# Optimization experiments

Measured on AMD Instinct MI355X. Metric: run time of the kernel, lower is better.

## Reference

```python
import jax, jax.numpy as jnp
import numpy as np

L, N, H, SQ = 24, 16384, 128, 32
D_OP, D_ATTR, D_FILT, D_OUT = 16, 56, 74, 32
D_IN = 2 * SQ + D_OP + D_ATTR  # 136
EPS = 1e-5
SLOPE = 0.01  # LeakyReLU default


def setup_inputs() -> dict:
    key = jax.random.key(0)
    ks = jax.random.split(key, 24)
    f32 = jnp.float32
    inp = {
        'op_pad': jax.random.normal(ks[0], (L, N, D_OP), f32),
        'attr_pad': jax.random.normal(ks[1], (L, N, D_ATTR), f32),
        'filter_pad': jax.random.normal(ks[2], (L, N, D_FILT), f32),
        'output_pad': jax.random.normal(ks[3], (L, N, D_OUT), f32),
        'mapping_pad': jax.random.randint(ks[4], (L, N, 2), 0, N + 1, jnp.int32),
        'batch_size': 4096,
        # filter / output squeeze linears
        'Wf': jax.random.normal(ks[5], (SQ, D_FILT), f32) * 0.05,
        'bf': jax.random.normal(ks[6], (SQ,), f32) * 0.05,
        'Wo': jax.random.normal(ks[7], (SQ, D_OUT), f32) * 0.05,
        'bo': jax.random.normal(ks[8], (SQ,), f32) * 0.05,
        # batchnorm affine params
        'g1': jnp.ones((SQ,), f32), 'beta1': jnp.zeros((SQ,), f32),
        'g2': jnp.ones((SQ,), f32), 'beta2': jnp.zeros((SQ,), f32),
        # LSTM (PyTorch layout: gates i,f,g,o stacked)
        'Wih': jax.random.normal(ks[9], (4 * H, D_IN), f32) * 0.05,
        'Whh': jax.random.normal(ks[10], (4 * H, H), f32) * 0.05,
        'bih': jax.random.normal(ks[11], (4 * H,), f32) * 0.05,
        'bhh': jax.random.normal(ks[12], (4 * H,), f32) * 0.05,
        # final MLP head
        'W1': jax.random.normal(ks[13], (20, H), f32) * 0.05,
        'b1': jax.random.normal(ks[14], (20,), f32) * 0.05,
        'W2': jax.random.normal(ks[15], (1, 20), f32) * 0.05,
        'b2': jax.random.normal(ks[16], (1,), f32) * 0.05,
    }
    return inp


def _leaky(x):
    return jnp.where(x > 0, x, SLOPE * x)


def _bn(x, g, b):
    # BatchNorm1d in training mode: batch stats (biased var), eps=1e-5
    m = jnp.mean(x, axis=0)
    v = jnp.var(x, axis=0)
    return (x - m) * jax.lax.rsqrt(v + EPS) * g + b


def _forward(op_pad, attr_pad, filter_pad, output_pad, mapping_pad, batch_size,
             Wf, bf, Wo, bo, g1, beta1, g2, beta2, Wih, Whh, bih, bhh, W1, b1, W2, b2):
    l, n = op_pad.shape[0], op_pad.shape[1]
    # squeeze filter / output features, flattened over (L*N)
    fd = _bn(_leaky(filter_pad.reshape(l * n, -1) @ Wf.T + bf), g1, beta1).reshape(l, n, SQ)
    od = _bn(_leaky(output_pad.reshape(l * n, -1) @ Wo.T + bo), g2, beta2).reshape(l, n, SQ)
    lstm_in = jnp.concatenate([op_pad, attr_pad, fd, od], axis=2)  # [L,N,D_IN]

    def step(carry, xs):
        h, c = carry                       # [N,H] previous level states
        x, mapping = xs                    # [N,D_IN], [N,2]
        mask = (mapping != 0)[..., None]   # [N,2,1]
        idx = jnp.maximum(mapping - 1, 0)  # [N,2] gather indices
        gh = jnp.sum(jnp.where(mask, h[idx], 0.0), axis=1) * 0.5  # [N,H]
        gc = jnp.sum(jnp.where(mask, c[idx], 0.0), axis=1) * 0.5
        gates = x @ Wih.T + bih + gh @ Whh.T + bhh  # [N,4H]
        i, f, g, o = jnp.split(gates, 4, axis=1)
        c_new = jax.nn.sigmoid(f) * gc + jax.nn.sigmoid(i) * jnp.tanh(g)
        h_new = jax.nn.sigmoid(o) * jnp.tanh(c_new)
        return (h_new, c_new), None

    z = jnp.zeros((n, H), lstm_in.dtype)
    # loop goes from the deepest level (index L-1) up to 0
    (h, _), _ = jax.lax.scan(step, (z, z), (lstm_in[::-1], mapping_pad[::-1]))
    out = h[:batch_size]
    out = jax.nn.sigmoid((out @ W1.T + b1) @ W2.T + b2)  # [B,1]
    return out


def reference(op_pad, attr_pad, filter_pad, output_pad, mapping_pad, batch_size,
              Wf, bf, Wo, bo, g1, beta1, g2, beta2, Wih, Whh, bih, bhh, W1, b1, W2, b2):
    return _forward(op_pad, attr_pad, filter_pad, output_pad, mapping_pad, batch_size,
                    Wf, bf, Wo, bo, g1, beta1, g2, beta2, Wih, Whh, bih, bhh, W1, b1, W2, b2)
```

## Files before the change

### kernel.cpp

```cpp
#include <hip/hip_runtime.h>
#include <hip/hip_bf16.h>

#define LL 24
#define NN 16384
#define HH 128
#define KP 288
#define LN (LL*NN)

typedef __bf16 bf16;
typedef __attribute__((ext_vector_type(8))) __bf16 bf16x8;
typedef __attribute__((ext_vector_type(4))) __bf16 bf16x4;
typedef __attribute__((ext_vector_type(2))) __bf16 bf16x2;
typedef __attribute__((ext_vector_type(4))) float f32x4;

__device__ __forceinline__ float sigm(float x){ return 1.f/(1.f+__expf(-x)); }
__device__ __forceinline__ float tanhfast(float x){
    float e = __expf(-2.f*fabsf(x));
    float t = (1.f-e)/(1.f+e);
    return x >= 0.f ? t : -t;
}
__device__ __forceinline__ void gld16(const void* g, void* l){
    __builtin_amdgcn_global_load_lds(
        (const __attribute__((address_space(1))) void*)g,
        (__attribute__((address_space(3))) void*)l, 16, 0, 0);
}

template<int D, int KQ>
__global__ void prep_wsplit(const float* __restrict__ W, bf16* __restrict__ Wsp)
{
    for (int idx = threadIdx.x; idx < KQ*256; idx += blockDim.x) {
        const int j   = idx & 7;
        const int col = (idx >> 3) & 31;
        const int kq  = idx >> 8;
        const int k   = kq*8 + j;
        float v = (k < D) ? W[col*D + k] : 0.f;
        bf16 h = (bf16)v;
        Wsp[idx]          = h;
        Wsp[KQ*256 + idx] = (bf16)(v - (float)h);
    }
}

template<int D, int KQ, int NQK>
__global__ __launch_bounds__(256) void act_mfma(
    const float* __restrict__ X, const bf16* __restrict__ Wsp,
    const float* __restrict__ bias, bf16* __restrict__ act,
    float* __restrict__ sums)
{
    constexpr int KSTEPS = KQ/4;
    constexpr int TILES  = LN/128;
    __shared__ __align__(16) bf16 XH[KQ*130*8];
    __shared__ __align__(16) bf16 XL[KQ*130*8];
    __shared__ float red[64];
    const int tid  = threadIdx.x;
    const int lane = tid & 63, w = tid >> 6;
    const int l15  = lane & 15, l4 = lane >> 4;

    if (tid < 64) red[tid] = 0.f;

    if constexpr (KQ > NQK) {
        for (int s = tid; s < (KQ-NQK)*128; s += 256) {
            const int kq = NQK + (s >> 7), r = s & 127;
            bf16x8 z;
            #pragma unroll
            for (int j=0;j<8;++j) z[j] = (bf16)0.f;
            *(bf16x8*)&XH[(kq*130 + r)*8] = z;
            *(bf16x8*)&XL[(kq*130 + r)*8] = z;
        }
    }

    bf16x8 wh[KSTEPS][2], wl[KSTEPS][2];
    #pragma unroll
    for (int ks=0; ks<KSTEPS; ++ks)
        #pragma unroll
        for (int cht=0; cht<2; ++cht) {
            const int idx = ((ks*4 + l4)*32 + cht*16 + l15)*8;
            wh[ks][cht] = *(const bf16x8*)&Wsp[idx];
            wl[ks][cht] = *(const bf16x8*)&Wsp[KQ*256 + idx];
        }
    float4 bb[2];
    #pragma unroll
    for (int cht=0; cht<2; ++cht) bb[cht] = *(const float4*)&bias[cht*16 + l4*4];

    float sst[2][4], ssq[2][4];
    #pragma unroll
    for (int c=0;c<2;++c)
        #pragma unroll
        for (int r=0;r<4;++r){ sst[c][r]=0.f; ssq[c][r]=0.f; }

    const int rowb = w*32;
    for (int tile = blockIdx.x; tile < TILES; tile += gridDim.x) {
        __syncthreads();
        const float* Xt = X + (size_t)tile*128*D;
        #pragma unroll
        for (int it = 0; it < (128*NQK)/256; ++it) {
            const int t = it*256 + tid;
            const int r = t / NQK, q = t - r*NQK;
            const float* src = Xt + (size_t)r*D + q*8;
            float xv[8];
            if constexpr (D % 8 != 0) {
                if (q == NQK-1) {
                    #pragma unroll
                    for (int j=0;j<8;++j) xv[j] = (j < D-(NQK-1)*8) ? src[j] : 0.f;
                } else {
                    float2 p0 = *(const float2*)(src);
                    float2 p1 = *(const float2*)(src+2);
                    float2 p2 = *(const float2*)(src+4);
                    float2 p3 = *(const float2*)(src+6);
                    xv[0]=p0.x; xv[1]=p0.y; xv[2]=p1.x; xv[3]=p1.y;
                    xv[4]=p2.x; xv[5]=p2.y; xv[6]=p3.x; xv[7]=p3.y;
                }
            } else {
                float4 f0 = *(const float4*)src;
                float4 f1 = *(const float4*)(src+4);
                xv[0]=f0.x; xv[1]=f0.y; xv[2]=f0.z; xv[3]=f0.w;
                xv[4]=f1.x; xv[5]=f1.y; xv[6]=f1.z; xv[7]=f1.w;
            }
            bf16x8 h8, l8;
            #pragma unroll
            for (int j=0;j<8;++j){
                float x = xv[j];
                bf16 hh = (bf16)x;
                h8[j] = hh;
                l8[j] = (bf16)(x - (float)hh);
            }
            const int slot = (q*130 + r)*8;
            *(bf16x8*)&XH[slot] = h8;
            *(bf16x8*)&XL[slot] = l8;
        }
        __syncthreads();

        f32x4 acc[2][2];
        #pragma unroll
        for (int cht=0; cht<2; ++cht)
            #pragma unroll
            for (int rt=0; rt<2; ++rt)
                acc[cht][rt] = (f32x4){bb[cht].x, bb[cht].y, bb[cht].z, bb[cht].w};

        #pragma unroll
        for (int ks=0; ks<KSTEPS; ++ks) {
            bf16x8 xh[2], xl[2];
            #pragma unroll
            for (int rt=0; rt<2; ++rt) {
                const int slot = ((ks*4 + l4)*130 + rowb + rt*16 + l15)*8;
                xh[rt] = *(const bf16x8*)&XH[slot];
                xl[rt] = *(const bf16x8*)&XL[slot];
            }
            #pragma unroll
            for (int cht=0; cht<2; ++cht)
                #pragma unroll
                for (int rt=0; rt<2; ++rt) {
                    acc[cht][rt] = __builtin_amdgcn_mfma_f32_16x16x32_bf16(
                        wh[ks][cht], xh[rt], acc[cht][rt], 0,0,0);
                    acc[cht][rt] = __builtin_amdgcn_mfma_f32_16x16x32_bf16(
                        wl[ks][cht], xh[rt], acc[cht][rt], 0,0,0);
                    acc[cht][rt] = __builtin_amdgcn_mfma_f32_16x16x32_bf16(
                        wh[ks][cht], xl[rt], acc[cht][rt], 0,0,0);
                }
        }

        #pragma unroll
        for (int cht=0; cht<2; ++cht)
            #pragma unroll
            for (int rt=0; rt<2; ++rt) {
                bf16x4 pk;
                #pragma unroll
                for (int reg=0; reg<4; ++reg) {
                    float u = acc[cht][rt][reg];
                    u = u > 0.f ? u : 0.01f*u;
                    pk[reg] = (bf16)u;
                    sst[cht][reg] += u;
                    ssq[cht][reg] += u*u;
                }
                const long row = (long)tile*128 + rowb + rt*16 + l15;
                *(bf16x4*)&act[row*32 + cht*16 + l4*4] = pk;
            }
    }

    __syncthreads();
    #pragma unroll
    for (int cht=0; cht<2; ++cht)
        #pragma unroll
        for (int reg=0; reg<4; ++reg) {
            const int ch = cht*16 + l4*4 + reg;
            atomicAdd(&red[ch],      sst[cht][reg]);
            atomicAdd(&red[32+ch],   ssq[cht][reg]);
        }
    __syncthreads();
    if (tid < 64) atomicAdd(&sums[tid], red[tid]);
}

__global__ void prep_wtb(const float* __restrict__ Wih, const float* __restrict__ Whh,
                         const float* __restrict__ bih, const float* __restrict__ bhh,
                         bf16* __restrict__ Wtb, float* __restrict__ b4p)
{
    const int np = blockIdx.x;
    const int k  = threadIdx.x;
    const int gate = (np>>4)&3;
    const int j = gate*128 + (np>>6)*16 + (np&15);
    if (k < KP) {
        float v = 0.f;
        if (k < 136)      v = Wih[(long)j*136 + k];
        else if (k >= 160) v = Whh[(long)j*128 + (k-160)];
        Wtb[(long)np*KP + k] = (bf16)v;
    }
    if (k == 0) b4p[np] = bih[j] + bhh[j];
}

__global__ void prep_stats(const float* __restrict__ stats,
    const float* __restrict__ g1, const float* __restrict__ beta1,
    const float* __restrict__ g2, const float* __restrict__ beta2,
    const float* __restrict__ W1, const float* __restrict__ b1,
    const float* __restrict__ W2, const float* __restrict__ b2,
    float* __restrict__ ss, float* __restrict__ wvb)
{
    const int t = threadIdx.x;
    const float inv = 1.f/(float)LN;
    if (t < 32) {
        float mean = stats[t]*inv;
        float var  = stats[32+t]*inv - mean*mean;
        float sc = g1[t]/sqrtf(var + 1e-5f);
        ss[t] = sc; ss[32+t] = beta1[t] - mean*sc;
    } else if (t < 64) {
        int c = t - 32;
        float mean = stats[64+c]*inv;
        float var  = stats[96+c]*inv - mean*mean;
        float sc = g2[c]/sqrtf(var + 1e-5f);
        ss[64+c] = sc; ss[96+c] = beta2[c] - mean*sc;
    }
    float s = 0.f;
    for (int a=0;a<20;++a) s += W2[a]*W1[a*HH + t];
    wvb[t] = s;
    if (t == 0) {
        float sb = 0.f;
        for (int a=0;a<20;++a) sb += W2[a]*b1[a];
        wvb[128] = sb + b2[0];
    }
}

__global__ __launch_bounds__(256) void build_a(
    const float* __restrict__ op, const float* __restrict__ attr,
    const bf16* __restrict__ actf, const bf16* __restrict__ acto,
    const int* __restrict__ map, const float* __restrict__ ss,
    const bf16* __restrict__ h_prev, bf16* __restrict__ A,
    int l, int first)
{
    const int n0 = blockIdx.x * 32;
    const long lbase = (long)l * NN;
    for (int i = threadIdx.x; i < 32*36; i += 256) {
        const int r = i / 36, c = i - r*36;
        const long n = n0 + r;
        const long e = lbase + n;
        const int k0 = c*8;
        bf16x8 out;
        if (c < 9) {
            const float* src = (c < 2) ? (op + e*16 + k0) : (attr + e*56 + (k0-16));
            float4 f0 = *(const float4*)src;
            float4 f1 = *(const float4*)(src+4);
            out[0]=(bf16)f0.x; out[1]=(bf16)f0.y; out[2]=(bf16)f0.z; out[3]=(bf16)f0.w;
            out[4]=(bf16)f1.x; out[5]=(bf16)f1.y; out[6]=(bf16)f1.z; out[7]=(bf16)f1.w;
        } else if (c < 17) {
            const int ch = (c < 13) ? (k0-72) : (k0-104);
            const bf16* src = (c < 13) ? (actf + e*32 + ch) : (acto + e*32 + ch);
            const float* s = ss + ((c < 13) ? 0 : 64);
            bf16x8 v = *(const bf16x8*)src;
            #pragma unroll
            for (int j=0;j<8;++j)
                out[j] = (bf16)fmaf((float)v[j], s[ch+j], s[32+ch+j]);
        } else if (c < 20) {
            #pragma unroll
            for (int j=0;j<8;++j) out[j] = (bf16)0.f;
        } else {
            const int jj = k0 - 160;
            float g[8] = {0,0,0,0,0,0,0,0};
            if (!first) {
                int2 mp = *(const int2*)&map[e*2];
                if (mp.x) { bf16x8 v = *(const bf16x8*)&h_prev[(long)(mp.x-1)*HH + jj];
                    #pragma unroll
                    for (int j=0;j<8;++j) g[j] += (float)v[j]; }
                if (mp.y) { bf16x8 v = *(const bf16x8*)&h_prev[(long)(mp.y-1)*HH + jj];
                    #pragma unroll
                    for (int j=0;j<8;++j) g[j] += (float)v[j]; }
            }
            #pragma unroll
            for (int j=0;j<8;++j) out[j] = (bf16)(0.5f*g[j]);
        }
        *(bf16x8*)&A[n*KP + k0] = out;
    }
}

__global__ __launch_bounds__(256) void lstm_gemm(
    const bf16* __restrict__ A, const bf16* __restrict__ Wtb,
    const float* __restrict__ b4p, const int* __restrict__ map,
    const float* __restrict__ c_prev, float* __restrict__ c_next,
    bf16* __restrict__ h_next, int l, int first)
{
    __shared__ bf16 As[128*32];
    __shared__ bf16 Bs[128*32];
    const int tid  = threadIdx.x;
    const int bm   = blockIdx.x;
    const int bn   = blockIdx.y;
    const int m0   = bm*128, n0p = bn*128;
    const int lane = tid & 63, w = tid >> 6;
    const int wr   = w >> 1,  wc = w & 1;

    f32x4 acc[4][4];
    #pragma unroll
    for (int ni=0; ni<4; ++ni){
        float b = b4p[n0p + wc*64 + ni*16 + (lane&15)];
        #pragma unroll
        for (int mi=0; mi<4; ++mi) acc[mi][ni] = (f32x4){b,b,b,b};
    }

    const bf16* Ab = A   + (size_t)m0*KP;
    const bf16* Bb = Wtb + (size_t)n0p*KP;
    const int lrr = lane >> 2;
    const int qs  = lane & 3;

    for (int kk=0; kk<9; ++kk){
        __syncthreads();
        #pragma unroll
        for (int hh=0; hh<2; ++hh){
            const int lr = w*32 + hh*16 + lrr;
            const int q  = qs ^ ((lr>>1)&3);
            const size_t go = (size_t)lr*KP + kk*32 + q*8;
            gld16(Ab + go, &As[(w*32 + hh*16)*32]);
            gld16(Bb + go, &Bs[(w*32 + hh*16)*32]);
        }
        __syncthreads();
        bf16x8 af[4], bfr[4];
        #pragma unroll
        for (int t4=0; t4<4; ++t4){
            const int am = wr*64 + t4*16 + (lane&15);
            af[t4] = *(const bf16x8*)&As[am*32 + (((lane>>4) ^ ((am>>1)&3))<<3)];
            const int bn_ = wc*64 + t4*16 + (lane&15);
            bfr[t4] = *(const bf16x8*)&Bs[bn_*32 + (((lane>>4) ^ ((bn_>>1)&3))<<3)];
        }
        #pragma unroll
        for (int mi=0; mi<4; ++mi)
            #pragma unroll
            for (int ni=0; ni<4; ++ni)
                acc[mi][ni] = __builtin_amdgcn_mfma_f32_16x16x32_bf16(
                    af[mi], bfr[ni], acc[mi][ni], 0, 0, 0);
    }

    const long lbase = (long)l * NN;
    const int cell = bn*32 + wc*16 + (lane&15);
    #pragma unroll
    for (int mi=0; mi<4; ++mi){
        const int rbase = m0 + wr*64 + mi*16 + (lane>>4)*4;
        #pragma unroll
        for (int reg=0; reg<4; ++reg){
            const int n = rbase + reg;
            float gc = 0.f;
            if (!first){
                int2 mp = *(const int2*)&map[(lbase+n)*2];
                if (mp.x) gc += c_prev[(long)(mp.x-1)*HH + cell];
                if (mp.y) gc += c_prev[(long)(mp.y-1)*HH + cell];
                gc *= 0.5f;
            }
            float cn = sigm(acc[mi][1][reg])*gc
                     + sigm(acc[mi][0][reg])*tanhfast(acc[mi][2][reg]);
            float hn = sigm(acc[mi][3][reg])*tanhfast(cn);
            c_next[(long)n*HH + cell] = cn;
            h_next[(long)n*HH + cell] = (bf16)hn;
        }
    }
}

__global__ __launch_bounds__(256) void final_k(
    const bf16* __restrict__ h, const float* __restrict__ wvb,
    float* __restrict__ out, int rows)
{
    int gt = blockIdx.x*256 + threadIdx.x;
    int row = gt >> 6;
    int lane = gt & 63;
    if (row >= rows) return;
    float v = fmaf((float)h[(long)row*HH + lane], wvb[lane],
                   (float)h[(long)row*HH + 64 + lane] * wvb[64+lane]);
    #pragma unroll
    for (int off=32; off>0; off>>=1) v += __shfl_down(v, off);
    if (lane == 0) out[row] = sigm(v + wvb[128]);
}

extern "C" void kernel_launch(void* const* d_in, const int* in_sizes, int n_in,
                              void* d_out, int out_size, void* d_ws, size_t ws_size,
                              hipStream_t stream)
{
    const float* op      = (const float*)d_in[0];
    const float* attr    = (const float*)d_in[1];
    const float* filt    = (const float*)d_in[2];
    const float* outp    = (const float*)d_in[3];
    const int*   mapping = (const int*)d_in[4];
    const float* Wf  = (const float*)d_in[6];
    const float* bf_ = (const float*)d_in[7];
    const float* Wo  = (const float*)d_in[8];
    const float* bo  = (const float*)d_in[9];
    const float* g1  = (const float*)d_in[10];
    const float* be1 = (const float*)d_in[11];
    const float* g2  = (const float*)d_in[12];
    const float* be2 = (const float*)d_in[13];
    const float* Wih = (const float*)d_in[14];
    const float* Whh = (const float*)d_in[15];
    const float* bih = (const float*)d_in[16];
    const float* bhh = (const float*)d_in[17];
    const float* W1  = (const float*)d_in[18];
    const float* b1  = (const float*)d_in[19];
    const float* W2  = (const float*)d_in[20];
    const float* b2  = (const float*)d_in[21];

    char* p = (char*)d_ws;
    auto alloc = [&](size_t bytes){ char* r = p; p += (bytes + 255) & ~255ull; return r; };
    bf16* actf = (bf16*)alloc((size_t)LN*32*2);
    bf16* acto = (bf16*)alloc((size_t)LN*32*2);
    bf16* h0   = (bf16*)alloc((size_t)NN*HH*2);
    bf16* h1   = (bf16*)alloc((size_t)NN*HH*2);
    float* c0  = (float*)alloc((size_t)NN*HH*4);
    float* c1  = (float*)alloc((size_t)NN*HH*4);
    bf16* Abuf = (bf16*)alloc((size_t)NN*KP*2);
    bf16* Wtb  = (bf16*)alloc((size_t)512*KP*2);
    float* b4p = (float*)alloc(512*4);
    float* stats=(float*)alloc(128*4);
    float* ssb = (float*)alloc(128*4);
    float* wvb = (float*)alloc(132*4);
    bf16* wspf = (bf16*)alloc((size_t)12*256*2*2);
    bf16* wspo = (bf16*)alloc((size_t)4*256*2*2);

    hipMemsetAsync(stats, 0, 128*sizeof(float), stream);
    prep_wsplit<74,12><<<1, 256, 0, stream>>>(Wf, wspf);
    prep_wsplit<32, 4><<<1, 256, 0, stream>>>(Wo, wspo);
    act_mfma<74,12,10><<<768, 256, 0, stream>>>(filt, wspf, bf_, actf, stats);
    act_mfma<32, 4, 4><<<1536, 256, 0, stream>>>(outp, wspo, bo, acto, stats+64);
    prep_wtb<<<512, 320, 0, stream>>>(Wih, Whh, bih, bhh, Wtb, b4p);
    prep_stats<<<1, 128, 0, stream>>>(stats, g1, be1, g2, be2, W1, b1, W2, b2, ssb, wvb);

    bf16*  hb[2] = {h0, h1};
    float* cb[2] = {c0, c1};
    for (int t = 0; t < LL; ++t) {
        const int l = (LL-1) - t;
        const int first = (t == 0);
        build_a<<<NN/32, 256, 0, stream>>>(op, attr, actf, acto, mapping, ssb,
                                           hb[t&1], Abuf, l, first);
        lstm_gemm<<<dim3(128,4), 256, 0, stream>>>(Abuf, Wtb, b4p, mapping,
            cb[t&1], cb[(t+1)&1], hb[(t+1)&1], l, first);
    }
    final_k<<<(out_size*64 + 255)/256, 256, 0, stream>>>(hb[0], wvb, (float*)d_out, out_size);
}
```

Measured before the change: 1.321 ms.

## Fuse LSTM input gather into GEMM, fold BN into weights, drop LDS staging

The per-level build_a kernel and its A buffer are removed. lstm_fused now loads op/attr/activation fragments and gathers child h states directly into MFMA operand registers, skipping the K-steps for h on the first level. The batchnorm scale and shift are folded into the Wih columns and the bias inside prep_wtb, which now runs after prep_stats. The squeeze-linear kernels also drop LDS staging and have each wave load its 16-row tile straight from global memory. This removes a global round trip and one launch per level, at the cost of uncoalesced direct global loads in the GEMM with no LDS reuse of the weights.

```diff
diff --git a/kernel.cpp b/kernel.cpp
--- a/kernel.cpp
+++ b/kernel.cpp
@@ -10,7 +10,6 @@
 typedef __bf16 bf16;
 typedef __attribute__((ext_vector_type(8))) __bf16 bf16x8;
 typedef __attribute__((ext_vector_type(4))) __bf16 bf16x4;
-typedef __attribute__((ext_vector_type(2))) __bf16 bf16x2;
 typedef __attribute__((ext_vector_type(4))) float f32x4;
 
 __device__ __forceinline__ float sigm(float x){ return 1.f/(1.f+__expf(-x)); }
@@ -18,11 +17,6 @@
     float e = __expf(-2.f*fabsf(x));
     float t = (1.f-e)/(1.f+e);
     return x >= 0.f ? t : -t;
-}
-__device__ __forceinline__ void gld16(const void* g, void* l){
-    __builtin_amdgcn_global_load_lds(
-        (const __attribute__((address_space(1))) void*)g,
-        (__attribute__((address_space(3))) void*)l, 16, 0, 0);
 }
 
 template<int D, int KQ>
@@ -40,16 +34,13 @@
     }
 }
 
-template<int D, int KQ, int NQK>
-__global__ __launch_bounds__(256) void act_mfma(
+template<int D, int KSTEPS>
+__global__ __launch_bounds__(256) void act_direct(
     const float* __restrict__ X, const bf16* __restrict__ Wsp,
     const float* __restrict__ bias, bf16* __restrict__ act,
     float* __restrict__ sums)
 {
-    constexpr int KSTEPS = KQ/4;
-    constexpr int TILES  = LN/128;
-    __shared__ __align__(16) bf16 XH[KQ*130*8];
-    __shared__ __align__(16) bf16 XL[KQ*130*8];
+    constexpr int KQ = KSTEPS*4;
     __shared__ float red[64];
     const int tid  = threadIdx.x;
     const int lane = tid & 63, w = tid >> 6;
@@ -57,17 +48,6 @@
 
     if (tid < 64) red[tid] = 0.f;
 
-    if constexpr (KQ > NQK) {
-        for (int s = tid; s < (KQ-NQK)*128; s += 256) {
-            const int kq = NQK + (s >> 7), r = s & 127;
-            bf16x8 z;
-            #pragma unroll
-            for (int j=0;j<8;++j) z[j] = (bf16)0.f;
-            *(bf16x8*)&XH[(kq*130 + r)*8] = z;
-            *(bf16x8*)&XL[(kq*130 + r)*8] = z;
-        }
-    }
-
     bf16x8 wh[KSTEPS][2], wl[KSTEPS][2];
     #pragma unroll
     for (int ks=0; ks<KSTEPS; ++ks)
@@ -87,93 +67,68 @@
         #pragma unroll
         for (int r=0;r<4;++r){ sst[c][r]=0.f; ssq[c][r]=0.f; }
 
-    const int rowb = w*32;
-    for (int tile = blockIdx.x; tile < TILES; tile += gridDim.x) {
-        __syncthreads();
-        const float* Xt = X + (size_t)tile*128*D;
-        #pragma unroll
-        for (int it = 0; it < (128*NQK)/256; ++it) {
-            const int t = it*256 + tid;
-            const int r = t / NQK, q = t - r*NQK;
-            const float* src = Xt + (size_t)r*D + q*8;
+    const int gw = blockIdx.x*4 + w, nw = gridDim.x*4;
+    for (int tile = gw; tile < LN/16; tile += nw) {
+        const long row = (long)tile*16 + l15;
+        const float* xp = X + row*D;
+
+        f32x4 acc[2];
+        #pragma unroll
+        for (int cht=0; cht<2; ++cht)
+            acc[cht] = (f32x4){bb[cht].x, bb[cht].y, bb[cht].z, bb[cht].w};
+
+        #pragma unroll
+        for (int ks=0; ks<KSTEPS; ++ks) {
+            const int k0 = ks*32 + l4*8;
             float xv[8];
-            if constexpr (D % 8 != 0) {
-                if (q == NQK-1) {
-                    #pragma unroll
-                    for (int j=0;j<8;++j) xv[j] = (j < D-(NQK-1)*8) ? src[j] : 0.f;
-                } else {
-                    float2 p0 = *(const float2*)(src);
-                    float2 p1 = *(const float2*)(src+2);
-                    float2 p2 = *(const float2*)(src+4);
-                    float2 p3 = *(const float2*)(src+6);
+            if constexpr (D % 32 == 0) {
+                float4 a = *(const float4*)(xp + k0);
+                float4 b = *(const float4*)(xp + k0 + 4);
+                xv[0]=a.x; xv[1]=a.y; xv[2]=a.z; xv[3]=a.w;
+                xv[4]=b.x; xv[5]=b.y; xv[6]=b.z; xv[7]=b.w;
+            } else {
+                const int rem = D - k0;
+                if (rem >= 8) {
+                    float2 p0 = *(const float2*)(xp + k0);
+                    float2 p1 = *(const float2*)(xp + k0 + 2);
+                    float2 p2 = *(const float2*)(xp + k0 + 4);
+                    float2 p3 = *(const float2*)(xp + k0 + 6);
                     xv[0]=p0.x; xv[1]=p0.y; xv[2]=p1.x; xv[3]=p1.y;
                     xv[4]=p2.x; xv[5]=p2.y; xv[6]=p3.x; xv[7]=p3.y;
+                } else {
+                    #pragma unroll
+                    for (int j=0;j<8;++j) xv[j] = (j < rem) ? xp[k0+j] : 0.f;
                 }
-            } else {
-                float4 f0 = *(const float4*)src;
-                float4 f1 = *(const float4*)(src+4);
-                xv[0]=f0.x; xv[1]=f0.y; xv[2]=f0.z; xv[3]=f0.w;
-                xv[4]=f1.x; xv[5]=f1.y; xv[6]=f1.z; xv[7]=f1.w;
-            }
-            bf16x8 h8, l8;
+            }
+            bf16x8 xh, xl;
             #pragma unroll
             for (int j=0;j<8;++j){
                 float x = xv[j];
                 bf16 hh = (bf16)x;
-                h8[j] = hh;
-                l8[j] = (bf16)(x - (float)hh);
-            }
-            const int slot = (q*130 + r)*8;
-            *(bf16x8*)&XH[slot] = h8;
-            *(bf16x8*)&XL[slot] = l8;
-        }
-        __syncthreads();
-
-        f32x4 acc[2][2];
-        #pragma unroll
-        for (int cht=0; cht<2; ++cht)
+                xh[j] = hh;
+                xl[j] = (bf16)(x - (float)hh);
+            }
             #pragma unroll
-            for (int rt=0; rt<2; ++rt)
-                acc[cht][rt] = (f32x4){bb[cht].x, bb[cht].y, bb[cht].z, bb[cht].w};
-
-        #pragma unroll
-        for (int ks=0; ks<KSTEPS; ++ks) {
-            bf16x8 xh[2], xl[2];
+            for (int cht=0; cht<2; ++cht) {
+                acc[cht] = __builtin_amdgcn_mfma_f32_16x16x32_bf16(wh[ks][cht], xh, acc[cht], 0,0,0);
+                acc[cht] = __builtin_amdgcn_mfma_f32_16x16x32_bf16(wl[ks][cht], xh, acc[cht], 0,0,0);
+                acc[cht] = __builtin_amdgcn_mfma_f32_16x16x32_bf16(wh[ks][cht], xl, acc[cht], 0,0,0);
+            }
+        }
+
+        #pragma unroll
+        for (int cht=0; cht<2; ++cht) {
+            bf16x4 pk;
             #pragma unroll
-            for (int rt=0; rt<2; ++rt) {
-                const int slot = ((ks*4 + l4)*130 + rowb + rt*16 + l15)*8;
-                xh[rt] = *(const bf16x8*)&XH[slot];
-                xl[rt] = *(const bf16x8*)&XL[slot];
-            }
-            #pragma unroll
-            for (int cht=0; cht<2; ++cht)
-                #pragma unroll
-                for (int rt=0; rt<2; ++rt) {
-                    acc[cht][rt] = __builtin_amdgcn_mfma_f32_16x16x32_bf16(
-                        wh[ks][cht], xh[rt], acc[cht][rt], 0,0,0);
-                    acc[cht][rt] = __builtin_amdgcn_mfma_f32_16x16x32_bf16(
-                        wl[ks][cht], xh[rt], acc[cht][rt], 0,0,0);
-                    acc[cht][rt] = __builtin_amdgcn_mfma_f32_16x16x32_bf16(
-                        wh[ks][cht], xl[rt], acc[cht][rt], 0,0,0);
-                }
-        }
-
-        #pragma unroll
-        for (int cht=0; cht<2; ++cht)
-            #pragma unroll
-            for (int rt=0; rt<2; ++rt) {
-                bf16x4 pk;
-                #pragma unroll
-                for (int reg=0; reg<4; ++reg) {
-                    float u = acc[cht][rt][reg];
-                    u = u > 0.f ? u : 0.01f*u;
-                    pk[reg] = (bf16)u;
-                    sst[cht][reg] += u;
-                    ssq[cht][reg] += u*u;
-                }
-                const long row = (long)tile*128 + rowb + rt*16 + l15;
-                *(bf16x4*)&act[row*32 + cht*16 + l4*4] = pk;
-            }
+            for (int reg=0; reg<4; ++reg) {
+                float u = acc[cht][reg];
+                u = u > 0.f ? u : 0.01f*u;
+                pk[reg] = (bf16)u;
+                sst[cht][reg] += u;
+                ssq[cht][reg] += u*u;
+            }
+            *(bf16x4*)&act[row*32 + cht*16 + l4*4] = pk;
+        }
     }
 
     __syncthreads();
@@ -182,28 +137,11 @@
         #pragma unroll
         for (int reg=0; reg<4; ++reg) {
             const int ch = cht*16 + l4*4 + reg;
-            atomicAdd(&red[ch],      sst[cht][reg]);
-            atomicAdd(&red[32+ch],   ssq[cht][reg]);
+            atomicAdd(&red[ch],    sst[cht][reg]);
+            atomicAdd(&red[32+ch], ssq[cht][reg]);
         }
     __syncthreads();
     if (tid < 64) atomicAdd(&sums[tid], red[tid]);
-}
-
-__global__ void prep_wtb(const float* __restrict__ Wih, const float* __restrict__ Whh,
-                         const float* __restrict__ bih, const float* __restrict__ bhh,
-                         bf16* __restrict__ Wtb, float* __restrict__ b4p)
-{
-    const int np = blockIdx.x;
-    const int k  = threadIdx.x;
-    const int gate = (np>>4)&3;
-    const int j = gate*128 + (np>>6)*16 + (np&15);
-    if (k < KP) {
-        float v = 0.f;
-        if (k < 136)      v = Wih[(long)j*136 + k];
-        else if (k >= 160) v = Whh[(long)j*128 + (k-160)];
-        Wtb[(long)np*KP + k] = (bf16)v;
-    }
-    if (k == 0) b4p[np] = bih[j] + bhh[j];
 }
 
 __global__ void prep_stats(const float* __restrict__ stats,
@@ -237,132 +175,179 @@
     }
 }
 
-__global__ __launch_bounds__(256) void build_a(
+__global__ void prep_wtb(const float* __restrict__ Wih, const float* __restrict__ Whh,
+                         const float* __restrict__ bih, const float* __restrict__ bhh,
+                         const float* __restrict__ ss,
+                         bf16* __restrict__ Wtb, float* __restrict__ b4p)
+{
+    const int np = blockIdx.x;
+    const int k  = threadIdx.x;
+    const int gate = (np>>4)&3;
+    const int j = gate*128 + (np>>6)*16 + (np&15);
+    if (k < KP) {
+        float v = 0.f;
+        if (k < 72)        v = Wih[(long)j*136 + k];
+        else if (k < 104)  v = Wih[(long)j*136 + k] * ss[k-72];
+        else if (k < 136)  v = Wih[(long)j*136 + k] * ss[64 + (k-104)];
+        else if (k >= 160) v = Whh[(long)j*128 + (k-160)];
+        Wtb[(long)np*KP + k] = (bf16)v;
+    }
+    if (k == 0) {
+        float b = bih[j] + bhh[j];
+        for (int c=0;c<32;++c) {
+            b += Wih[(long)j*136 + 72 + c]  * ss[32+c];
+            b += Wih[(long)j*136 + 104 + c] * ss[96+c];
+        }
+        b4p[np] = b;
+    }
+}
+
+__global__ __launch_bounds__(256) void lstm_fused(
     const float* __restrict__ op, const float* __restrict__ attr,
     const bf16* __restrict__ actf, const bf16* __restrict__ acto,
-    const int* __restrict__ map, const float* __restrict__ ss,
-    const bf16* __restrict__ h_prev, bf16* __restrict__ A,
-    int l, int first)
-{
-    const int n0 = blockIdx.x * 32;
-    const long lbase = (long)l * NN;
-    for (int i = threadIdx.x; i < 32*36; i += 256) {
-        const int r = i / 36, c = i - r*36;
-        const long n = n0 + r;
-        const long e = lbase + n;
-        const int k0 = c*8;
-        bf16x8 out;
-        if (c < 9) {
-            const float* src = (c < 2) ? (op + e*16 + k0) : (attr + e*56 + (k0-16));
-            float4 f0 = *(const float4*)src;
-            float4 f1 = *(const float4*)(src+4);
-            out[0]=(bf16)f0.x; out[1]=(bf16)f0.y; out[2]=(bf16)f0.z; out[3]=(bf16)f0.w;
-            out[4]=(bf16)f1.x; out[5]=(bf16)f1.y; out[6]=(bf16)f1.z; out[7]=(bf16)f1.w;
-        } else if (c < 17) {
-            const int ch = (c < 13) ? (k0-72) : (k0-104);
-            const bf16* src = (c < 13) ? (actf + e*32 + ch) : (acto + e*32 + ch);
-            const float* s = ss + ((c < 13) ? 0 : 64);
-            bf16x8 v = *(const bf16x8*)src;
-            #pragma unroll
-            for (int j=0;j<8;++j)
-                out[j] = (bf16)fmaf((float)v[j], s[ch+j], s[32+ch+j]);
-        } else if (c < 20) {
-            #pragma unroll
-            for (int j=0;j<8;++j) out[j] = (bf16)0.f;
-        } else {
-            const int jj = k0 - 160;
-            float g[8] = {0,0,0,0,0,0,0,0};
-            if (!first) {
-                int2 mp = *(const int2*)&map[e*2];
-                if (mp.x) { bf16x8 v = *(const bf16x8*)&h_prev[(long)(mp.x-1)*HH + jj];
-                    #pragma unroll
-                    for (int j=0;j<8;++j) g[j] += (float)v[j]; }
-                if (mp.y) { bf16x8 v = *(const bf16x8*)&h_prev[(long)(mp.y-1)*HH + jj];
-                    #pragma unroll
-                    for (int j=0;j<8;++j) g[j] += (float)v[j]; }
-            }
-            #pragma unroll
-            for (int j=0;j<8;++j) out[j] = (bf16)(0.5f*g[j]);
-        }
-        *(bf16x8*)&A[n*KP + k0] = out;
-    }
-}
-
-__global__ __launch_bounds__(256) void lstm_gemm(
-    const bf16* __restrict__ A, const bf16* __restrict__ Wtb,
-    const float* __restrict__ b4p, const int* __restrict__ map,
+    const bf16* __restrict__ Wtb, const float* __restrict__ b4p,
+    const int* __restrict__ map, const bf16* __restrict__ h_prev,
     const float* __restrict__ c_prev, float* __restrict__ c_next,
     bf16* __restrict__ h_next, int l, int first)
 {
-    __shared__ bf16 As[128*32];
-    __shared__ bf16 Bs[128*32];
     const int tid  = threadIdx.x;
-    const int bm   = blockIdx.x;
-    const int bn   = blockIdx.y;
-    const int m0   = bm*128, n0p = bn*128;
     const int lane = tid & 63, w = tid >> 6;
     const int wr   = w >> 1,  wc = w & 1;
+    const int l15  = lane & 15, l4 = lane >> 4;
+    const int bm   = blockIdx.x, bn = blockIdx.y;
+    const int m0   = bm*128, n0p = bn*128;
+    const long lbase = (long)l * NN;
 
     f32x4 acc[4][4];
     #pragma unroll
     for (int ni=0; ni<4; ++ni){
-        float b = b4p[n0p + wc*64 + ni*16 + (lane&15)];
+        float b = b4p[n0p + wc*64 + ni*16 + l15];
         #pragma unroll
         for (int mi=0; mi<4; ++mi) acc[mi][ni] = (f32x4){b,b,b,b};
     }
 
-    const bf16* Ab = A   + (size_t)m0*KP;
-    const bf16* Bb = Wtb + (size_t)n0p*KP;
-    const int lrr = lane >> 2;
-    const int qs  = lane & 3;
-
-    for (int kk=0; kk<9; ++kk){
-        __syncthreads();
-        #pragma unroll
-        for (int hh=0; hh<2; ++hh){
-            const int lr = w*32 + hh*16 + lrr;
-            const int q  = qs ^ ((lr>>1)&3);
-            const size_t go = (size_t)lr*KP + kk*32 + q*8;
-            gld16(Ab + go, &As[(w*32 + hh*16)*32]);
-            gld16(Bb + go, &Bs[(w*32 + hh*16)*32]);
-        }
-        __syncthreads();
-        bf16x8 af[4], bfr[4];
-        #pragma unroll
-        for (int t4=0; t4<4; ++t4){
-            const int am = wr*64 + t4*16 + (lane&15);
-            af[t4] = *(const bf16x8*)&As[am*32 + (((lane>>4) ^ ((am>>1)&3))<<3)];
-            const int bn_ = wc*64 + t4*16 + (lane&15);
-            bfr[t4] = *(const bf16x8*)&Bs[bn_*32 + (((lane>>4) ^ ((bn_>>1)&3))<<3)];
-        }
+    int2 mp_l; mp_l.x = 0; mp_l.y = 0;
+    if (!first) mp_l = *(const int2*)&map[(lbase + m0 + wr*64 + lane)*2];
+
+    const long e0 = lbase + m0 + wr*64 + l15;
+    const bf16* Bb[4];
+    #pragma unroll
+    for (int ni=0; ni<4; ++ni)
+        Bb[ni] = Wtb + (size_t)(n0p + wc*64 + ni*16 + l15)*KP + l4*8;
+
+    auto f32frag = [](const float* p) -> bf16x8 {
+        float4 a = *(const float4*)p, b = *(const float4*)(p+4);
+        bf16x8 r;
+        r[0]=(bf16)a.x; r[1]=(bf16)a.y; r[2]=(bf16)a.z; r[3]=(bf16)a.w;
+        r[4]=(bf16)b.x; r[5]=(bf16)b.y; r[6]=(bf16)b.z; r[7]=(bf16)b.w;
+        return r;
+    };
+
+    bf16x8 af[4], bfr[4];
+    auto loadB = [&](int kk){
+        #pragma unroll
+        for (int ni=0; ni<4; ++ni) bfr[ni] = *(const bf16x8*)(Bb[ni] + kk*32);
+    };
+    auto mfma16 = [&](){
         #pragma unroll
         for (int mi=0; mi<4; ++mi)
             #pragma unroll
             for (int ni=0; ni<4; ++ni)
                 acc[mi][ni] = __builtin_amdgcn_mfma_f32_16x16x32_bf16(
                     af[mi], bfr[ni], acc[mi][ni], 0, 0, 0);
-    }
-
-    const long lbase = (long)l * NN;
-    const int cell = bn*32 + wc*16 + (lane&15);
-    #pragma unroll
-    for (int mi=0; mi<4; ++mi){
-        const int rbase = m0 + wr*64 + mi*16 + (lane>>4)*4;
+    };
+
+    loadB(0);
+    #pragma unroll
+    for (int mi=0; mi<4; ++mi){
+        const long e = e0 + mi*16;
+        af[mi] = (l4 < 2) ? f32frag(op + e*16 + l4*8)
+                          : f32frag(attr + e*56 + (l4-2)*8);
+    }
+    mfma16();
+    loadB(1);
+    #pragma unroll
+    for (int mi=0; mi<4; ++mi){
+        const long e = e0 + mi*16;
+        af[mi] = f32frag(attr + e*56 + 16 + l4*8);
+    }
+    mfma16();
+    loadB(2);
+    #pragma unroll
+    for (int mi=0; mi<4; ++mi){
+        const long e = e0 + mi*16;
+        af[mi] = (l4 == 0) ? f32frag(attr + e*56 + 48)
+                           : *(const bf16x8*)(actf + e*32 + (l4-1)*8);
+    }
+    mfma16();
+    loadB(3);
+    #pragma unroll
+    for (int mi=0; mi<4; ++mi){
+        const long e = e0 + mi*16;
+        af[mi] = (l4 == 0) ? *(const bf16x8*)(actf + e*32 + 24)
+                           : *(const bf16x8*)(acto + e*32 + (l4-1)*8);
+    }
+    mfma16();
+    loadB(4);
+    #pragma unroll
+    for (int mi=0; mi<4; ++mi){
+        const long e = e0 + mi*16;
+        if (l4 == 0) af[mi] = *(const bf16x8*)(acto + e*32 + 24);
+        else { bf16x8 z; 
+               #pragma unroll
+               for (int j=0;j<8;++j) z[j]=(bf16)0.f; af[mi]=z; }
+    }
+    mfma16();
+    if (!first) {
+        #pragma unroll
+        for (int kk=5; kk<9; ++kk){
+            loadB(kk);
+            const int koff = (kk-5)*32 + l4*8;
+            #pragma unroll
+            for (int mi=0; mi<4; ++mi){
+                const int src = mi*16 + l15;
+                const int px = __shfl(mp_l.x, src);
+                const int py = __shfl(mp_l.y, src);
+                float g[8] = {0.f,0.f,0.f,0.f,0.f,0.f,0.f,0.f};
+                if (px) {
+                    bf16x8 v = *(const bf16x8*)&h_prev[(long)(px-1)*HH + koff];
+                    #pragma unroll
+                    for (int j=0;j<8;++j) g[j] += (float)v[j];
+                }
+                if (py) {
+                    bf16x8 v = *(const bf16x8*)&h_prev[(long)(py-1)*HH + koff];
+                    #pragma unroll
+                    for (int j=0;j<8;++j) g[j] += (float)v[j];
+                }
+                bf16x8 r;
+                #pragma unroll
+                for (int j=0;j<8;++j) r[j] = (bf16)(0.5f*g[j]);
+                af[mi] = r;
+            }
+            mfma16();
+        }
+    }
+
+    const int cell = bn*32 + wc*16 + l15;
+    #pragma unroll
+    for (int mi=0; mi<4; ++mi){
         #pragma unroll
         for (int reg=0; reg<4; ++reg){
-            const int n = rbase + reg;
+            const int rloc = mi*16 + l4*4 + reg;
+            const long n = m0 + wr*64 + rloc;
             float gc = 0.f;
             if (!first){
-                int2 mp = *(const int2*)&map[(lbase+n)*2];
-                if (mp.x) gc += c_prev[(long)(mp.x-1)*HH + cell];
-                if (mp.y) gc += c_prev[(long)(mp.y-1)*HH + cell];
+                const int px = __shfl(mp_l.x, rloc);
+                const int py = __shfl(mp_l.y, rloc);
+                if (px) gc += c_prev[(long)(px-1)*HH + cell];
+                if (py) gc += c_prev[(long)(py-1)*HH + cell];
                 gc *= 0.5f;
             }
             float cn = sigm(acc[mi][1][reg])*gc
                      + sigm(acc[mi][0][reg])*tanhfast(acc[mi][2][reg]);
             float hn = sigm(acc[mi][3][reg])*tanhfast(cn);
-            c_next[(long)n*HH + cell] = cn;
-            h_next[(long)n*HH + cell] = (bf16)hn;
+            c_next[n*HH + cell] = cn;
+            h_next[n*HH + cell] = (bf16)hn;
         }
     }
 }
@@ -416,7 +401,6 @@
     bf16* h1   = (bf16*)alloc((size_t)NN*HH*2);
     float* c0  = (float*)alloc((size_t)NN*HH*4);
     float* c1  = (float*)alloc((size_t)NN*HH*4);
-    bf16* Abuf = (bf16*)alloc((size_t)NN*KP*2);
     bf16* Wtb  = (bf16*)alloc((size_t)512*KP*2);
     float* b4p = (float*)alloc(512*4);
     float* stats=(float*)alloc(128*4);
@@ -428,19 +412,18 @@
     hipMemsetAsync(stats, 0, 128*sizeof(float), stream);
     prep_wsplit<74,12><<<1, 256, 0, stream>>>(Wf, wspf);
     prep_wsplit<32, 4><<<1, 256, 0, stream>>>(Wo, wspo);
-    act_mfma<74,12,10><<<768, 256, 0, stream>>>(filt, wspf, bf_, actf, stats);
-    act_mfma<32, 4, 4><<<1536, 256, 0, stream>>>(outp, wspo, bo, acto, stats+64);
-    prep_wtb<<<512, 320, 0, stream>>>(Wih, Whh, bih, bhh, Wtb, b4p);
+    act_direct<74,3><<<1024, 256, 0, stream>>>(filt, wspf, bf_, actf, stats);
+    act_direct<32,1><<<1024, 256, 0, stream>>>(outp, wspo, bo, acto, stats+64);
     prep_stats<<<1, 128, 0, stream>>>(stats, g1, be1, g2, be2, W1, b1, W2, b2, ssb, wvb);
+    prep_wtb<<<512, 320, 0, stream>>>(Wih, Whh, bih, bhh, ssb, Wtb, b4p);
 
     bf16*  hb[2] = {h0, h1};
     float* cb[2] = {c0, c1};
     for (int t = 0; t < LL; ++t) {
         const int l = (LL-1) - t;
         const int first = (t == 0);
-        build_a<<<NN/32, 256, 0, stream>>>(op, attr, actf, acto, mapping, ssb,
-                                           hb[t&1], Abuf, l, first);
-        lstm_gemm<<<dim3(128,4), 256, 0, stream>>>(Abuf, Wtb, b4p, mapping,
+        lstm_fused<<<dim3(128,4), 256, 0, stream>>>(op, attr, actf, acto,
+            Wtb, b4p, mapping, hb[t&1],
             cb[t&1], cb[(t+1)&1], hb[(t+1)&1], l, first);
     }
     final_k<<<(out_size*64 + 255)/256, 256, 0, stream>>>(hb[0], wvb, (float*)d_out, out_size);
```

Result: no change. 1.340 ms (+1.4%).
